# Performance work log

Measured on AMD Instinct MI355X. Metric: run time of the kernel, lower is better.

Reference implementation:

```python
import jax, jax.numpy as jnp
import numpy as np

N, X_DIM, Y_DIM, HID = 1024, 128, 128, 256


def setup_inputs() -> dict:
    key = jax.random.key(0)
    k1, k2, k3, k4 = jax.random.split(key, 4)
    return {
        "x_samples": jax.random.normal(k1, (N, X_DIM), dtype=jnp.float32),
        "y_samples": jax.random.normal(k2, (N, Y_DIM), dtype=jnp.float32),
        "W1": jax.random.normal(k3, (X_DIM + Y_DIM, HID), dtype=jnp.float32) * 0.05,
        "b1": jnp.zeros((HID,), dtype=jnp.float32),
        "W2": jax.random.normal(k4, (HID, 1), dtype=jnp.float32) * 0.05,
        "b2": jnp.zeros((1,), dtype=jnp.float32),
    }


def reference(x_samples, y_samples, W1, b1, W2, b2):
    n = y_samples.shape[0]
    x_dim = x_samples.shape[-1]
    # Split first linear so we never materialize the N^2 concat:
    W1x, W1y = W1[:x_dim], W1[x_dim:]
    pre_x = x_samples @ W1x  # [N, H]
    pre_y = y_samples @ W1y  # [N, H]
    # T0: F on matched pairs (x_i, y_i)
    T0 = jax.nn.relu(pre_x + pre_y + b1) @ W2 + b2  # [N, 1]
    # T1[i, j] = F([x_j, y_i]) - 1.0  (all-pairs grid)
    h = jax.nn.relu(pre_x[None, :, :] + pre_y[:, None, :] + b1)  # [N, N, H]
    T1 = h @ W2 + b2 - 1.0  # [N, N, 1]
    lse = jax.nn.logsumexp(T1, axis=1)  # [N, 1]
    lower_bound = T0.mean() - jnp.exp(lse - jnp.log(jnp.float32(n))).mean()
    return lower_bound
```

## Files before the change

kernel.cpp:

```cpp
#include <hip/hip_runtime.h>

typedef _Float16 h2 __attribute__((ext_vector_type(2)));
typedef unsigned int u32;

#define OFF_XP   0u
#define OFF_YP   0x40000u
#define OFF_W1XP 0x80000u
#define OFF_W1YP 0x90000u
#define OFF_W2H  0xA0000u
#define OFF_A2   0x100000u
#define OFF_C2   0x180000u

__device__ __forceinline__ u32 pack2(float a, float b) {
  h2 v; v.x = (_Float16)a; v.y = (_Float16)b;
  return __builtin_bit_cast(u32, v);
}
__device__ __forceinline__ h2 as_h2(u32 u) { return __builtin_bit_cast(h2, u); }

__device__ __forceinline__ float fdot2(h2 a, h2 b, float c) {
#if __has_builtin(__builtin_amdgcn_fdot2)
  return __builtin_amdgcn_fdot2(a, b, c, false);
#else
  return (float)a.x * (float)b.x + (float)a.y * (float)b.y + c;
#endif
}
__device__ __forceinline__ h2 relu2(h2 t) {
  h2 z; z.x = (_Float16)0.0f; z.y = (_Float16)0.0f;
  return __builtin_elementwise_max(t, z);
}

__global__ void k0_pack(const float* __restrict__ x, const float* __restrict__ y,
                        const float* __restrict__ W1, const float* __restrict__ W2,
                        u32* __restrict__ wsu) {
  const int b = blockIdx.x, tid = threadIdx.x;
  if (b < 128) {
    const float* src = (b < 64) ? x : y;
    u32* dst = wsu + ((b < 64) ? (OFF_XP >> 2) : (OFF_YP >> 2));
    const int bb = b & 63, kt = bb & 3, rt = bb >> 2;
    __shared__ float sT[64][33];
    const int kl = tid & 31, rg = tid >> 5;
#pragma unroll
    for (int p = 0; p < 8; ++p) {
      const int r = p * 8 + rg;
      sT[r][kl] = src[(rt * 64 + r) * 128 + kt * 32 + kl];
    }
    __syncthreads();
    const int rl = tid & 63, kg = tid >> 6;
#pragma unroll
    for (int q = 0; q < 4; ++q) {
      const int kkl = q * 4 + kg;
      dst[(kt * 16 + kkl) * 1024 + rt * 64 + rl] =
          pack2(sT[rl][2 * kkl], sT[rl][2 * kkl + 1]);
    }
  } else if (b < 192) {
    const int kk = b - 128, h = tid;
    wsu[(OFF_W1XP >> 2) + kk * 256 + h] =
        pack2(W1[(2 * kk) * 256 + h], W1[(2 * kk + 1) * 256 + h]);
    wsu[(OFF_W1YP >> 2) + kk * 256 + h] =
        pack2(W1[(128 + 2 * kk) * 256 + h], W1[(129 + 2 * kk) * 256 + h]);
  } else {
    if (tid < 128) wsu[(OFF_W2H >> 2) + tid] = pack2(W2[2 * tid], W2[2 * tid + 1]);
  }
}

__global__ __launch_bounds__(256) void k1_pre(u32* __restrict__ wsu,
                                              const float* __restrict__ b1) {
  const int b = blockIdx.x, tid = threadIdx.x;
  const int mat = b >> 8;
  const int bb = b & 255, ht = bb & 7, rt = bb >> 3;
  const int tx = tid & 31, ty = tid >> 5;
  const int h0 = ht * 32 + ty * 4;
  const u32* xp  = wsu + (mat ? (OFF_YP >> 2) : (OFF_XP >> 2)) + rt * 32 + tx;
  const u32* w1p = wsu + (mat ? (OFF_W1YP >> 2) : (OFF_W1XP >> 2)) + h0;
  u32* dst = wsu + (mat ? (OFF_C2 >> 2) : (OFF_A2 >> 2)) + rt * 4096 + tx;

  float acc[4];
  if (mat) {
    const float4 bv = *(const float4*)(b1 + h0);
    acc[0] = bv.x; acc[1] = bv.y; acc[2] = bv.z; acc[3] = bv.w;
  } else {
    acc[0] = acc[1] = acc[2] = acc[3] = 0.0f;
  }

  u32 XR[8]; uint4 WR[8];
#pragma unroll
  for (int s = 0; s < 8; ++s) {
    XR[s] = xp[s * 1024];
    WR[s] = *(const uint4*)(w1p + s * 256);
  }
#pragma unroll 8
  for (int kk = 0; kk < 56; ++kk) {
    const int s = kk & 7;
    const h2 xr = as_h2(XR[s]); const uint4 wv = WR[s];
    XR[s] = xp[(kk + 8) * 1024];
    WR[s] = *(const uint4*)(w1p + (kk + 8) * 256);
    acc[0] = fdot2(xr, as_h2(wv.x), acc[0]);
    acc[1] = fdot2(xr, as_h2(wv.y), acc[1]);
    acc[2] = fdot2(xr, as_h2(wv.z), acc[2]);
    acc[3] = fdot2(xr, as_h2(wv.w), acc[3]);
  }
#pragma unroll
  for (int kk = 56; kk < 64; ++kk) {
    const int s = kk & 7;
    const h2 xr = as_h2(XR[s]); const uint4 wv = WR[s];
    acc[0] = fdot2(xr, as_h2(wv.x), acc[0]);
    acc[1] = fdot2(xr, as_h2(wv.y), acc[1]);
    acc[2] = fdot2(xr, as_h2(wv.z), acc[2]);
    acc[3] = fdot2(xr, as_h2(wv.w), acc[3]);
  }
  const int hh0 = h0 >> 1;
  dst[hh0 * 32]       = pack2(acc[0], acc[1]);
  dst[(hh0 + 1) * 32] = pack2(acc[2], acc[3]);
}

__global__ __launch_bounds__(256) void k2_main(const u32* __restrict__ wsu,
                                               const float* __restrict__ B2,
                                               float* __restrict__ out) {
  const int bi = blockIdx.x >> 5, bj = blockIdx.x & 31;
  const int tid = threadIdx.x;
  const int tx = tid & 15, ty = tid >> 4;
  const u32* pa = wsu + (OFF_A2 >> 2) + bj * 4096 + tx * 2;
  const u32* pc = wsu + (OFF_C2 >> 2) + bi * 4096 + ty * 2;

  __shared__ u32 sw[128];
  __shared__ float sred[4];
  if (tid < 128) sw[tid] = wsu[(OFF_W2H >> 2) + tid];
  __syncthreads();

  float acc[4] = {0.0f, 0.0f, 0.0f, 0.0f};
  uint2 A[8], C[8]; u32 W[8];
#pragma unroll
  for (int s = 0; s < 8; ++s) {
    A[s] = *(const uint2*)(pa + s * 32);
    C[s] = *(const uint2*)(pc + s * 32);
    W[s] = sw[s];
  }
#pragma unroll 8
  for (int hh = 0; hh < 120; ++hh) {
    const int s = hh & 7;
    const uint2 av = A[s], cv = C[s];
    const h2 w = as_h2(W[s]);
    A[s] = *(const uint2*)(pa + (hh + 8) * 32);
    C[s] = *(const uint2*)(pc + (hh + 8) * 32);
    W[s] = sw[hh + 8];
    const h2 a0 = as_h2(av.x), a1 = as_h2(av.y);
    const h2 c0 = as_h2(cv.x), c1 = as_h2(cv.y);
    acc[0] = fdot2(relu2(a0 + c0), w, acc[0]);
    acc[1] = fdot2(relu2(a1 + c0), w, acc[1]);
    acc[2] = fdot2(relu2(a0 + c1), w, acc[2]);
    acc[3] = fdot2(relu2(a1 + c1), w, acc[3]);
  }
#pragma unroll
  for (int hh = 120; hh < 128; ++hh) {
    const int s = hh & 7;
    const uint2 av = A[s], cv = C[s];
    const h2 w = as_h2(W[s]);
    const h2 a0 = as_h2(av.x), a1 = as_h2(av.y);
    const h2 c0 = as_h2(cv.x), c1 = as_h2(cv.y);
    acc[0] = fdot2(relu2(a0 + c0), w, acc[0]);
    acc[1] = fdot2(relu2(a1 + c0), w, acc[1]);
    acc[2] = fdot2(relu2(a0 + c1), w, acc[2]);
    acc[3] = fdot2(relu2(a1 + c1), w, acc[3]);
  }

  const float b2 = B2[0];
  float val = 0.0f;
#pragma unroll
  for (int p = 0; p < 4; ++p) val += __expf(acc[p] + (b2 - 1.0f));
  val *= -1.0f / 1048576.0f;
  if (bi == bj && tx == ty)
    val += (acc[0] + acc[3] + 2.0f * b2) * (1.0f / 1024.0f);
#pragma unroll
  for (int off = 32; off > 0; off >>= 1) val += __shfl_down(val, off, 64);
  if ((tid & 63) == 0) sred[tid >> 6] = val;
  __syncthreads();
  if (tid == 0) atomicAdd(out, sred[0] + sred[1] + sred[2] + sred[3]);
}

extern "C" void kernel_launch(void* const* d_in, const int* in_sizes, int n_in,
                              void* d_out, int out_size, void* d_ws, size_t ws_size,
                              hipStream_t stream) {
  const float* x  = (const float*)d_in[0];
  const float* y  = (const float*)d_in[1];
  const float* W1 = (const float*)d_in[2];
  const float* b1 = (const float*)d_in[3];
  const float* W2 = (const float*)d_in[4];
  const float* b2 = (const float*)d_in[5];
  u32* wsu = (u32*)d_ws;

  hipMemsetAsync(d_out, 0, sizeof(float), stream);
  hipLaunchKernelGGL(k0_pack, dim3(193), dim3(256), 0, stream, x, y, W1, W2, wsu);
  hipLaunchKernelGGL(k1_pre, dim3(512), dim3(256), 0, stream, wsu, b1);
  hipLaunchKernelGGL(k2_main, dim3(1024), dim3(256), 0, stream, wsu, b2, (float*)d_out);
}
```

Before: 107.7 us.

## Stage pre-activation tiles in swizzled LDS and drop memset launch

The intermediate A/C layout becomes row-major per sample, with 128 packed h2 per row, so k1 writes uint2 per thread. k2_main loads 32x128 tiles of A and C into XOR-swizzled shared memory with 16-byte loads, then runs its inner loop from LDS instead of strided global loads held in a register pipeline. The output zeroing moves into k0_pack, which removes the hipMemsetAsync call, and W2 packing moves into k2. The cost is 32KB of LDS per block, which may lower occupancy, plus an extra sync.

```diff
diff --git a/kernel.cpp b/kernel.cpp
--- a/kernel.cpp
+++ b/kernel.cpp
@@ -7,7 +7,6 @@
 #define OFF_YP   0x40000u
 #define OFF_W1XP 0x80000u
 #define OFF_W1YP 0x90000u
-#define OFF_W2H  0xA0000u
 #define OFF_A2   0x100000u
 #define OFF_C2   0x180000u
 
@@ -30,9 +29,10 @@
 }
 
 __global__ void k0_pack(const float* __restrict__ x, const float* __restrict__ y,
-                        const float* __restrict__ W1, const float* __restrict__ W2,
-                        u32* __restrict__ wsu) {
+                        const float* __restrict__ W1, u32* __restrict__ wsu,
+                        float* __restrict__ out) {
   const int b = blockIdx.x, tid = threadIdx.x;
+  if (b == 0 && tid == 0) out[0] = 0.0f;
   if (b < 128) {
     const float* src = (b < 64) ? x : y;
     u32* dst = wsu + ((b < 64) ? (OFF_XP >> 2) : (OFF_YP >> 2));
@@ -52,14 +52,12 @@
       dst[(kt * 16 + kkl) * 1024 + rt * 64 + rl] =
           pack2(sT[rl][2 * kkl], sT[rl][2 * kkl + 1]);
     }
-  } else if (b < 192) {
+  } else {
     const int kk = b - 128, h = tid;
     wsu[(OFF_W1XP >> 2) + kk * 256 + h] =
         pack2(W1[(2 * kk) * 256 + h], W1[(2 * kk + 1) * 256 + h]);
     wsu[(OFF_W1YP >> 2) + kk * 256 + h] =
         pack2(W1[(128 + 2 * kk) * 256 + h], W1[(129 + 2 * kk) * 256 + h]);
-  } else {
-    if (tid < 128) wsu[(OFF_W2H >> 2) + tid] = pack2(W2[2 * tid], W2[2 * tid + 1]);
   }
 }
 
@@ -72,7 +70,7 @@
   const int h0 = ht * 32 + ty * 4;
   const u32* xp  = wsu + (mat ? (OFF_YP >> 2) : (OFF_XP >> 2)) + rt * 32 + tx;
   const u32* w1p = wsu + (mat ? (OFF_W1YP >> 2) : (OFF_W1XP >> 2)) + h0;
-  u32* dst = wsu + (mat ? (OFF_C2 >> 2) : (OFF_A2 >> 2)) + rt * 4096 + tx;
+  u32* dst = wsu + (mat ? (OFF_C2 >> 2) : (OFF_A2 >> 2)) + rt * 4096 + tx * 128;
 
   float acc[4];
   if (mat) {
@@ -108,59 +106,68 @@
     acc[2] = fdot2(xr, as_h2(wv.z), acc[2]);
     acc[3] = fdot2(xr, as_h2(wv.w), acc[3]);
   }
-  const int hh0 = h0 >> 1;
-  dst[hh0 * 32]       = pack2(acc[0], acc[1]);
-  dst[(hh0 + 1) * 32] = pack2(acc[2], acc[3]);
+  const int hh0 = ht * 16 + ty * 2;
+  uint2 sv;
+  sv.x = pack2(acc[0], acc[1]);
+  sv.y = pack2(acc[2], acc[3]);
+  *(uint2*)(dst + hh0) = sv;
 }
 
 __global__ __launch_bounds__(256) void k2_main(const u32* __restrict__ wsu,
+                                               const float* __restrict__ W2g,
                                                const float* __restrict__ B2,
                                                float* __restrict__ out) {
   const int bi = blockIdx.x >> 5, bj = blockIdx.x & 31;
   const int tid = threadIdx.x;
   const int tx = tid & 15, ty = tid >> 4;
-  const u32* pa = wsu + (OFF_A2 >> 2) + bj * 4096 + tx * 2;
-  const u32* pc = wsu + (OFF_C2 >> 2) + bi * 4096 + ty * 2;
-
-  __shared__ u32 sw[128];
+
+  __shared__ uint4 sA4[32 * 32];
+  __shared__ uint4 sC4[32 * 32];
+  __shared__ uint4 sW4[32];
   __shared__ float sred[4];
-  if (tid < 128) sw[tid] = wsu[(OFF_W2H >> 2) + tid];
+  u32* sW2 = (u32*)sW4;
+
+  {
+    const u32* gA = wsu + (OFF_A2 >> 2) + bj * 4096;
+    const u32* gC = wsu + (OFF_C2 >> 2) + bi * 4096;
+    const int j = tid >> 3, q8 = tid & 7, sw = (j >> 1) & 7;
+#pragma unroll
+    for (int m = 0; m < 4; ++m) {
+      const int q = q8 + 8 * m;
+      sA4[j * 32 + (q ^ sw)] = *(const uint4*)(gA + j * 128 + q * 4);
+      sC4[j * 32 + (q ^ sw)] = *(const uint4*)(gC + j * 128 + q * 4);
+    }
+    if (tid < 128) sW2[tid] = pack2(W2g[2 * tid], W2g[2 * tid + 1]);
+  }
   __syncthreads();
 
+  const uint4* rA0 = sA4 + (2 * tx) * 32;
+  const uint4* rA1 = rA0 + 32;
+  const uint4* rC0 = sC4 + (2 * ty) * 32;
+  const uint4* rC1 = rC0 + 32;
+  const int swzA = tx & 7, swzC = ty & 7;
+
   float acc[4] = {0.0f, 0.0f, 0.0f, 0.0f};
-  uint2 A[8], C[8]; u32 W[8];
-#pragma unroll
-  for (int s = 0; s < 8; ++s) {
-    A[s] = *(const uint2*)(pa + s * 32);
-    C[s] = *(const uint2*)(pc + s * 32);
-    W[s] = sw[s];
-  }
-#pragma unroll 8
-  for (int hh = 0; hh < 120; ++hh) {
-    const int s = hh & 7;
-    const uint2 av = A[s], cv = C[s];
-    const h2 w = as_h2(W[s]);
-    A[s] = *(const uint2*)(pa + (hh + 8) * 32);
-    C[s] = *(const uint2*)(pc + (hh + 8) * 32);
-    W[s] = sw[hh + 8];
-    const h2 a0 = as_h2(av.x), a1 = as_h2(av.y);
-    const h2 c0 = as_h2(cv.x), c1 = as_h2(cv.y);
-    acc[0] = fdot2(relu2(a0 + c0), w, acc[0]);
-    acc[1] = fdot2(relu2(a1 + c0), w, acc[1]);
-    acc[2] = fdot2(relu2(a0 + c1), w, acc[2]);
-    acc[3] = fdot2(relu2(a1 + c1), w, acc[3]);
-  }
-#pragma unroll
-  for (int hh = 120; hh < 128; ++hh) {
-    const int s = hh & 7;
-    const uint2 av = A[s], cv = C[s];
-    const h2 w = as_h2(W[s]);
-    const h2 a0 = as_h2(av.x), a1 = as_h2(av.y);
-    const h2 c0 = as_h2(cv.x), c1 = as_h2(cv.y);
-    acc[0] = fdot2(relu2(a0 + c0), w, acc[0]);
-    acc[1] = fdot2(relu2(a1 + c0), w, acc[1]);
-    acc[2] = fdot2(relu2(a0 + c1), w, acc[2]);
-    acc[3] = fdot2(relu2(a1 + c1), w, acc[3]);
+#pragma unroll 4
+  for (int g = 0; g < 32; ++g) {
+    const uint4 av0 = rA0[g ^ swzA], av1 = rA1[g ^ swzA];
+    const uint4 cv0 = rC0[g ^ swzC], cv1 = rC1[g ^ swzC];
+    const uint4 wv = sW4[g];
+    const u32 a0[4] = {av0.x, av0.y, av0.z, av0.w};
+    const u32 a1[4] = {av1.x, av1.y, av1.z, av1.w};
+    const u32 c0[4] = {cv0.x, cv0.y, cv0.z, cv0.w};
+    const u32 c1[4] = {cv1.x, cv1.y, cv1.z, cv1.w};
+    const u32 ww[4] = {wv.x, wv.y, wv.z, wv.w};
+#pragma unroll
+    for (int m = 0; m < 4; ++m) {
+      const h2 A0 = as_h2(a0[m]), A1 = as_h2(a1[m]);
+      const h2 C0 = as_h2(c0[m]), C1 = as_h2(c1[m]);
+      const h2 w = as_h2(ww[m]);
+      acc[0] = fdot2(relu2(A0 + C0), w, acc[0]);
+      acc[1] = fdot2(relu2(A1 + C0), w, acc[1]);
+      acc[2] = fdot2(relu2(A0 + C1), w, acc[2]);
+      acc[3] = fdot2(relu2(A1 + C1), w, acc[3]);
+    }
   }
 
   const float b2 = B2[0];
@@ -188,8 +195,9 @@
   const float* b2 = (const float*)d_in[5];
   u32* wsu = (u32*)d_ws;
 
-  hipMemsetAsync(d_out, 0, sizeof(float), stream);
-  hipLaunchKernelGGL(k0_pack, dim3(193), dim3(256), 0, stream, x, y, W1, W2, wsu);
+  hipLaunchKernelGGL(k0_pack, dim3(192), dim3(256), 0, stream, x, y, W1, wsu,
+                     (float*)d_out);
   hipLaunchKernelGGL(k1_pre, dim3(512), dim3(256), 0, stream, wsu, b1);
-  hipLaunchKernelGGL(k2_main, dim3(1024), dim3(256), 0, stream, wsu, b2, (float*)d_out);
-}
+  hipLaunchKernelGGL(k2_main, dim3(1024), dim3(256), 0, stream, wsu, W2, b2,
+                     (float*)d_out);
+}
```

Result: faster. 91.52 us (-15.0%).
